# Optimization experiments

Hardware: AMD Instinct MI355X
Metric: run time of the kernel (lower is better)

## Reference

```python
import jax, jax.numpy as jnp
import numpy as np

B, N, K_NB, C, KERNEL, OUT = 32, 128, 16, 1024, 8, 1024
TWO_PI = 2.0 * np.pi
EPS = 1e-14


def setup_inputs() -> dict:
    key = jax.random.key(0)
    ks = jax.random.split(key, 9)
    return {
        "node_feats": jax.random.normal(ks[0], (B, N, C), dtype=jnp.float32),
        "node_centre": jax.random.uniform(ks[1], (B, N, 2), dtype=jnp.float32),
        "neighbor_idx": jax.random.randint(ks[2], (B, N, K_NB), 0, N, dtype=jnp.int32),
        "graph_weights": jax.random.uniform(ks[3], (B, N, K_NB), dtype=jnp.float32),
        "mean_rho": jax.random.uniform(ks[4], (1, KERNEL), dtype=jnp.float32),
        "mean_theta": jax.random.uniform(ks[5], (1, KERNEL), minval=-np.pi, maxval=np.pi, dtype=jnp.float32),
        "precision_rho": jax.random.uniform(ks[6], (1, KERNEL), dtype=jnp.float32),
        "precision_theta": jax.random.uniform(ks[7], (1, KERNEL), dtype=jnp.float32),
        "conv_w": jax.random.normal(ks[8], (KERNEL, C, OUT // KERNEL), dtype=jnp.float32) * 0.02,
    }


def _gaussian_weights(node_centre, neighbor_idx, mean_rho, mean_theta, precision_rho, precision_theta):
    # gather neighbor centres per batch: [B,N,K,2]
    centre_j = jax.vmap(lambda c, idx: c[idx])(node_centre, neighbor_idx)
    diff = node_centre[:, :, None, :] - centre_j           # node_i - node_j
    cx, cy = diff[..., 0], diff[..., 1]                    # chunk order: x first
    rho = jnp.sqrt(cx ** 2 + cy ** 2)                      # [B,N,K]
    theta = jnp.arctan2(cx, cy)                            # note: atan2(x, y) as in source
    d_rho = (rho[..., None] - mean_rho[0]) ** 2            # [B,N,K,KERNEL]
    w_rho = jnp.exp(-0.5 * d_rho / (EPS + precision_rho[0] ** 2))
    a1 = jnp.abs(theta[..., None] - mean_theta[0])
    a2 = jnp.abs(TWO_PI - a1)
    w_theta = jnp.exp(-0.5 * jnp.minimum(a1, a2) ** 2 / (EPS + precision_theta[0] ** 2))
    w = w_rho * w_theta
    w = jnp.where(jnp.isnan(w), 0.0, w)
    return w / jnp.sum(w, axis=-1, keepdims=True)          # normalize over kernel dim


def reference(node_feats, node_centre, neighbor_idx, graph_weights,
              mean_rho, mean_theta, precision_rho, precision_theta, conv_w):
    gw = _gaussian_weights(node_centre, neighbor_idx, mean_rho, mean_theta,
                           precision_rho, precision_theta)       # [B,N,K,KERNEL]
    edge_w = graph_weights[..., None] * gw                        # use_graph_weights=True
    # gather neighbor features per batch: [B,N,K,C]
    feats_j = jax.vmap(lambda f, idx: f[idx])(node_feats, neighbor_idx)
    # bmm aggregation: [B,N,KERNEL,C]
    agg = jnp.einsum('bnkm,bnkc->bnmc', edge_w, feats_j)
    # per-kernel linear (no bias) then concat: [B,N,KERNEL,OUT//KERNEL] -> [B,N,OUT]
    out = jnp.einsum('bnmc,mcd->bnmd', agg, conv_w)
    out = out.reshape(node_feats.shape[0], node_feats.shape[1], -1)
    return jax.nn.relu(out)
```

## Files before the change

kernel.cpp:

```cpp
#include <hip/hip_runtime.h>
#include <hip/hip_bf16.h>

#define B_   32
#define N_   128
#define KNB  16
#define C_   1024
#define KER  8
#define DOUT 128
#define OUTC 1024

typedef __attribute__((ext_vector_type(8))) short bf16x8;
typedef __attribute__((ext_vector_type(4))) float f32x4;

__device__ __forceinline__ ushort f2bf(float f) {
    unsigned u = __builtin_bit_cast(unsigned, f);
    unsigned r = (u + 0x7FFFu + ((u >> 16) & 1u)) >> 16;
    return (ushort)r;
}

__global__ __launch_bounds__(256) void k_prep(const float* __restrict__ f,
                                              ushort* __restrict__ Fb,
                                              const float* __restrict__ cw,
                                              ushort* __restrict__ WbT,
                                              const float* __restrict__ centre,
                                              const int* __restrict__ nidx,
                                              const float* __restrict__ gw,
                                              const float* __restrict__ mr,
                                              const float* __restrict__ mt,
                                              const float* __restrict__ pr,
                                              const float* __restrict__ pt,
                                              float* __restrict__ ew) {
    __shared__ float tile[32][33];
    int bid = blockIdx.x;
    int tid = threadIdx.x;
    if (bid < 4096) {
        int t = bid * 256 + tid;
        float4 v = ((const float4*)f)[t];
        ushort4 o;
        o.x = f2bf(v.x); o.y = f2bf(v.y); o.z = f2bf(v.z); o.w = f2bf(v.w);
        ((ushort4*)Fb)[t] = o;
    } else if (bid < 5120) {
        int b2 = bid - 4096;
        int dt = b2 & 3;
        int ct = (b2 >> 2) & 31;
        int m  = b2 >> 7;
        int tx = tid & 31;
        int ty = tid >> 5;
#pragma unroll
        for (int i = 0; i < 4; ++i) {
            int cr = ty + i * 8;
            tile[cr][tx] = cw[((size_t)m * C_ + (ct * 32 + cr)) * DOUT + dt * 32 + tx];
        }
        __syncthreads();
#pragma unroll
        for (int i = 0; i < 4; ++i) {
            int dr = ty + i * 8;
            WbT[((size_t)(m * DOUT + dt * 32 + dr)) * C_ + ct * 32 + tx] = f2bf(tile[tx][dr]);
        }
    } else {
        int t = (bid - 5120) * 256 + tid;
        int bn = t >> 4;
        int b  = bn >> 7;
        float2 ci = *(const float2*)(centre + (size_t)bn * 2);
        int j = nidx[t];
        float2 cj = *(const float2*)(centre + (size_t)(b * N_ + j) * 2);
        float cx = ci.x - cj.x, cy = ci.y - cj.y;
        float rho = sqrtf(cx * cx + cy * cy);
        float theta = atan2f(cx, cy);
        float w[KER];
        float sum = 0.f;
#pragma unroll
        for (int m = 0; m < KER; ++m) {
            float dr = rho - mr[m];
            float wr = expf(-0.5f * dr * dr / (1e-14f + pr[m] * pr[m]));
            float a1 = fabsf(theta - mt[m]);
            float a2 = fabsf(6.2831853071795864f - a1);
            float am = fminf(a1, a2);
            float wt = expf(-0.5f * am * am / (1e-14f + pt[m] * pt[m]));
            float wv = wr * wt;
            if (isnan(wv)) wv = 0.f;
            w[m] = wv;
            sum += wv;
        }
        float scale = gw[t] / sum;
#pragma unroll
        for (int m = 0; m < KER; ++m) ew[(size_t)t * KER + m] = w[m] * scale;
    }
}

__global__ __launch_bounds__(512, 2) void k_fused(const ushort* __restrict__ Fb,
                                                  const ushort* __restrict__ WbT,
                                                  const float* __restrict__ ew,
                                                  const int* __restrict__ nidx,
                                                  float* __restrict__ out) {
    __shared__ float Gt[128 * 132];

    int tid  = threadIdx.x;
    int wave = tid >> 6;
    int lane = tid & 63;
    int kq = wave >> 2;
    int rh = (wave >> 1) & 1;
    int ch = wave & 1;
    int lr = lane & 15;
    int kg = lane >> 4;
    int bid = blockIdx.x;
    int b = bid & 31;
    int m = bid >> 5;

    const ushort* Ab = Fb  + ((size_t)(b * N_ + rh * 64 + lr)) * C_ + kq * 512 + kg * 8;
    const ushort* Bb = WbT + ((size_t)(m * DOUT + ch * 64 + lr)) * C_ + kq * 512 + kg * 8;

    f32x4 acc[4][4];
#pragma unroll
    for (int i = 0; i < 4; ++i)
#pragma unroll
        for (int j = 0; j < 4; ++j) acc[i][j] = (f32x4){0.f, 0.f, 0.f, 0.f};

#pragma unroll
    for (int s = 0; s < 16; ++s) {
        bf16x8 av[4], bv[4];
#pragma unroll
        for (int i = 0; i < 4; ++i) {
            av[i] = *(const bf16x8*)(Ab + (size_t)i * 16 * C_ + s * 32);
            bv[i] = *(const bf16x8*)(Bb + (size_t)i * 16 * C_ + s * 32);
        }
#pragma unroll
        for (int mi = 0; mi < 4; ++mi)
#pragma unroll
            for (int nj = 0; nj < 4; ++nj)
                acc[mi][nj] = __builtin_amdgcn_mfma_f32_16x16x32_bf16(
                    av[mi], bv[nj], acc[mi][nj], 0, 0, 0);
    }

    int n = tid >> 2, q = tid & 3;
    const int* ip = nidx + (size_t)(b * N_ + n) * KNB;
    int4 jv0 = *(const int4*)(ip);
    int4 jv1 = *(const int4*)(ip + 4);
    int4 jv2 = *(const int4*)(ip + 8);
    int4 jv3 = *(const int4*)(ip + 12);
    const float* ep = ew + (size_t)(b * N_ + n) * (KNB * KER) + m;
    float wv[KNB];
#pragma unroll
    for (int k = 0; k < KNB; ++k) wv[k] = ep[k * KER];

    if (kq == 0) {
#pragma unroll
        for (int mi = 0; mi < 4; ++mi)
#pragma unroll
            for (int nj = 0; nj < 4; ++nj)
#pragma unroll
                for (int r = 0; r < 4; ++r) {
                    int grow = rh * 64 + mi * 16 + kg * 4 + r;
                    int gcol = ch * 64 + nj * 16 + lr;
                    Gt[grow * 132 + gcol] = acc[mi][nj][r];
                }
    }
    __syncthreads();
    if (kq == 1) {
#pragma unroll
        for (int mi = 0; mi < 4; ++mi)
#pragma unroll
            for (int nj = 0; nj < 4; ++nj)
#pragma unroll
                for (int r = 0; r < 4; ++r) {
                    int grow = rh * 64 + mi * 16 + kg * 4 + r;
                    int gcol = ch * 64 + nj * 16 + lr;
                    Gt[grow * 132 + gcol] += acc[mi][nj][r];
                }
    }
    __syncthreads();

    int rot[8];
#pragma unroll
    for (int i = 0; i < 8; ++i) rot[i] = (q * 4 + i * 4) & 31;
    f32x4 o[8];
#pragma unroll
    for (int i = 0; i < 8; ++i) o[i] = (f32x4){0.f, 0.f, 0.f, 0.f};
    int jarr[KNB] = {jv0.x, jv0.y, jv0.z, jv0.w, jv1.x, jv1.y, jv1.z, jv1.w,
                     jv2.x, jv2.y, jv2.z, jv2.w, jv3.x, jv3.y, jv3.z, jv3.w};
#pragma unroll
    for (int k = 0; k < KNB; ++k) {
        const float* gr = Gt + jarr[k] * 132 + q * 32;
        float w = wv[k];
#pragma unroll
        for (int i = 0; i < 8; ++i) {
            f32x4 v = *(const f32x4*)(gr + rot[i]);
            o[i] += v * w;
        }
    }
    float* op = out + (size_t)(b * N_ + n) * OUTC + m * DOUT + q * 32;
#pragma unroll
    for (int i = 0; i < 8; ++i) {
        f32x4 r = o[i];
#pragma unroll
        for (int jj = 0; jj < 4; ++jj) r[jj] = fmaxf(r[jj], 0.f);
        *(f32x4*)(op + rot[i]) = r;
    }
}

extern "C" void kernel_launch(void* const* d_in, const int* in_sizes, int n_in,
                              void* d_out, int out_size, void* d_ws, size_t ws_size,
                              hipStream_t stream) {
    const float* node_feats      = (const float*)d_in[0];
    const float* node_centre     = (const float*)d_in[1];
    const int*   neighbor_idx    = (const int*)d_in[2];
    const float* graph_weights   = (const float*)d_in[3];
    const float* mean_rho        = (const float*)d_in[4];
    const float* mean_theta      = (const float*)d_in[5];
    const float* precision_rho   = (const float*)d_in[6];
    const float* precision_theta = (const float*)d_in[7];
    const float* conv_w          = (const float*)d_in[8];
    float* out = (float*)d_out;

    char* ws = (char*)d_ws;
    ushort* Fb  = (ushort*)(ws);
    ushort* WbT = (ushort*)(ws + (8u  << 20));
    float*  ew  = (float*) (ws + (10u << 20));

    k_prep<<<5376, 256, 0, stream>>>(node_feats, Fb, conv_w, WbT,
                                     node_centre, neighbor_idx, graph_weights,
                                     mean_rho, mean_theta,
                                     precision_rho, precision_theta, ew);
    k_fused<<<256, 512, 0, stream>>>(Fb, WbT, ew, neighbor_idx, out);
}
```

Baseline: 130.8 us.

## Pack bf16 features and weights in MFMA fragment order for coalesced loads

The prep kernel now writes node features and conv weights into a lane-ordered packed layout, staged through shared memory. Each wave's MFMA operand loads in the fused kernel become fully contiguous 1KB reads instead of strided row reads. Prep work is regrouped into fewer, larger blocks (576 instead of 5376), so each block does more per-thread work. The trade-off is extra LDS traffic and reduced parallelism in the prep kernel.

```diff
diff --git a/kernel.cpp b/kernel.cpp
--- a/kernel.cpp
+++ b/kernel.cpp
@@ -18,10 +18,11 @@
     return (ushort)r;
 }
 
-__global__ __launch_bounds__(256) void k_prep(const float* __restrict__ f,
-                                              ushort* __restrict__ Fb,
-                                              const float* __restrict__ cw,
-                                              ushort* __restrict__ WbT,
+
+__global__ __launch_bounds__(256) void k_prep(const float* __restrict__ F,
+                                              ushort* __restrict__ Fpack,
+                                              const float* __restrict__ W,
+                                              ushort* __restrict__ Wpack,
                                               const float* __restrict__ centre,
                                               const int* __restrict__ nidx,
                                               const float* __restrict__ gw,
@@ -30,39 +31,58 @@
                                               const float* __restrict__ pr,
                                               const float* __restrict__ pt,
                                               float* __restrict__ ew) {
-    __shared__ float tile[32][33];
+    __shared__ ushort Pt[16 * 1032];
     int bid = blockIdx.x;
-    int tid = threadIdx.x;
-    if (bid < 4096) {
-        int t = bid * 256 + tid;
-        float4 v = ((const float4*)f)[t];
-        ushort4 o;
-        o.x = f2bf(v.x); o.y = f2bf(v.y); o.z = f2bf(v.z); o.w = f2bf(v.w);
-        ((ushort4*)Fb)[t] = o;
-    } else if (bid < 5120) {
-        int b2 = bid - 4096;
-        int dt = b2 & 3;
-        int ct = (b2 >> 2) & 31;
-        int m  = b2 >> 7;
-        int tx = tid & 31;
-        int ty = tid >> 5;
-#pragma unroll
-        for (int i = 0; i < 4; ++i) {
-            int cr = ty + i * 8;
-            tile[cr][tx] = cw[((size_t)m * C_ + (ct * 32 + cr)) * DOUT + dt * 32 + tx];
+    int t   = threadIdx.x;
+
+    if (bid < 256) {
+        int R0 = bid * 16;
+#pragma unroll
+        for (int it = 0; it < 16; ++it) {
+            float4 v = *(const float4*)(F + (size_t)(R0 + it) * C_ + t * 4);
+            ushort* d = Pt + it * 1032 + t * 4;
+            d[0] = f2bf(v.x); d[1] = f2bf(v.y); d[2] = f2bf(v.z); d[3] = f2bf(v.w);
         }
         __syncthreads();
-#pragma unroll
-        for (int i = 0; i < 4; ++i) {
-            int dr = ty + i * 8;
-            WbT[((size_t)(m * DOUT + dt * 32 + dr)) * C_ + ct * 32 + tx] = f2bf(tile[tx][dr]);
+        ushort* dst = Fpack + (size_t)bid * 16384;
+#pragma unroll
+        for (int it = 0; it < 8; ++it) {
+            int c  = it * 256 + t;
+            int ln = c & 63, s = (c >> 6) & 15, kq = c >> 10;
+            int lr = ln & 15, kg = ln >> 4;
+            bf16x8 v = *(const bf16x8*)(Pt + lr * 1032 + kq * 512 + s * 32 + kg * 8);
+            *(bf16x8*)(dst + (size_t)c * 8) = v;
+        }
+    } else if (bid < 320) {
+        int b2 = bid - 256;
+        int m  = b2 >> 3;
+        int D0 = ((b2 >> 2) & 1) * 64 + (b2 & 3) * 16;
+#pragma unroll
+        for (int it = 0; it < 16; ++it) {
+            int f  = it * 256 + t;
+            int c  = f >> 2, q4 = f & 3;
+            float4 v = *(const float4*)(W + (size_t)m * (C_ * DOUT) + (size_t)c * DOUT + D0 + q4 * 4);
+            Pt[(q4 * 4 + 0) * 1032 + c] = f2bf(v.x);
+            Pt[(q4 * 4 + 1) * 1032 + c] = f2bf(v.y);
+            Pt[(q4 * 4 + 2) * 1032 + c] = f2bf(v.z);
+            Pt[(q4 * 4 + 3) * 1032 + c] = f2bf(v.w);
+        }
+        __syncthreads();
+        ushort* dst = Wpack + (size_t)b2 * 16384;
+#pragma unroll
+        for (int it = 0; it < 8; ++it) {
+            int c  = it * 256 + t;
+            int ln = c & 63, s = (c >> 6) & 15, kq = c >> 10;
+            int lr = ln & 15, kg = ln >> 4;
+            bf16x8 v = *(const bf16x8*)(Pt + lr * 1032 + kq * 512 + s * 32 + kg * 8);
+            *(bf16x8*)(dst + (size_t)c * 8) = v;
         }
     } else {
-        int t = (bid - 5120) * 256 + tid;
-        int bn = t >> 4;
+        int tt = (bid - 320) * 256 + t;
+        int bn = tt >> 4;
         int b  = bn >> 7;
         float2 ci = *(const float2*)(centre + (size_t)bn * 2);
-        int j = nidx[t];
+        int j = nidx[tt];
         float2 cj = *(const float2*)(centre + (size_t)(b * N_ + j) * 2);
         float cx = ci.x - cj.x, cy = ci.y - cj.y;
         float rho = sqrtf(cx * cx + cy * cy);
@@ -82,14 +102,14 @@
             w[m] = wv;
             sum += wv;
         }
-        float scale = gw[t] / sum;
-#pragma unroll
-        for (int m = 0; m < KER; ++m) ew[(size_t)t * KER + m] = w[m] * scale;
-    }
-}
-
-__global__ __launch_bounds__(512, 2) void k_fused(const ushort* __restrict__ Fb,
-                                                  const ushort* __restrict__ WbT,
+        float scale = gw[tt] / sum;
+#pragma unroll
+        for (int m = 0; m < KER; ++m) ew[(size_t)tt * KER + m] = w[m] * scale;
+    }
+}
+
+__global__ __launch_bounds__(512, 2) void k_fused(const ushort* __restrict__ Fpack,
+                                                  const ushort* __restrict__ Wpack,
                                                   const float* __restrict__ ew,
                                                   const int* __restrict__ nidx,
                                                   float* __restrict__ out) {
@@ -107,8 +127,13 @@
     int b = bid & 31;
     int m = bid >> 5;
 
-    const ushort* Ab = Fb  + ((size_t)(b * N_ + rh * 64 + lr)) * C_ + kq * 512 + kg * 8;
-    const ushort* Bb = WbT + ((size_t)(m * DOUT + ch * 64 + lr)) * C_ + kq * 512 + kg * 8;
+    const ushort* Abase[4];
+    const ushort* Bbase[4];
+#pragma unroll
+    for (int i = 0; i < 4; ++i) {
+        Abase[i] = Fpack + ((size_t)(b * 8 + rh * 4 + i) * 16384 + kq * 8192 + lane * 8);
+        Bbase[i] = Wpack + ((size_t)(m * 8 + ch * 4 + i) * 16384 + kq * 8192 + lane * 8);
+    }
 
     f32x4 acc[4][4];
 #pragma unroll
@@ -121,8 +146,8 @@
         bf16x8 av[4], bv[4];
 #pragma unroll
         for (int i = 0; i < 4; ++i) {
-            av[i] = *(const bf16x8*)(Ab + (size_t)i * 16 * C_ + s * 32);
-            bv[i] = *(const bf16x8*)(Bb + (size_t)i * 16 * C_ + s * 32);
+            av[i] = *(const bf16x8*)(Abase[i] + s * 512);
+            bv[i] = *(const bf16x8*)(Bbase[i] + s * 512);
         }
 #pragma unroll
         for (int mi = 0; mi < 4; ++mi)
@@ -213,13 +238,13 @@
     float* out = (float*)d_out;
 
     char* ws = (char*)d_ws;
-    ushort* Fb  = (ushort*)(ws);
-    ushort* WbT = (ushort*)(ws + (8u  << 20));
-    float*  ew  = (float*) (ws + (10u << 20));
-
-    k_prep<<<5376, 256, 0, stream>>>(node_feats, Fb, conv_w, WbT,
-                                     node_centre, neighbor_idx, graph_weights,
-                                     mean_rho, mean_theta,
-                                     precision_rho, precision_theta, ew);
-    k_fused<<<256, 512, 0, stream>>>(Fb, WbT, ew, neighbor_idx, out);
-}
+    ushort* Fpack = (ushort*)(ws);
+    ushort* Wpack = (ushort*)(ws + (8u  << 20));
+    float*  ew    = (float*) (ws + (10u << 20));
+
+    k_prep<<<576, 256, 0, stream>>>(node_feats, Fpack, conv_w, Wpack,
+                                    node_centre, neighbor_idx, graph_weights,
+                                    mean_rho, mean_theta,
+                                    precision_rho, precision_theta, ew);
+    k_fused<<<256, 512, 0, stream>>>(Fpack, Wpack, ew, neighbor_idx, out);
+}
```

After: 108.1 us. -17.4%, faster.
